# Kernel optimization log

Hardware: AMD Instinct MI355X
Metric: run time of the kernel (lower is better)

The kernel has to match this reference:

```python
import jax, jax.numpy as jnp
import numpy as np
from jax import lax

B, N, D = 2, 2048, 1024
H = 16
DH = D // H
EXP = 4
INNER = EXP * D
KS = 3
POWER = 2
LN_EPS = 1e-5


def _layer_norm(x, g, b):
    mu = jnp.mean(x, axis=-1, keepdims=True)
    var = jnp.mean(jnp.square(x - mu), axis=-1, keepdims=True)
    return (x - mu) * lax.rsqrt(var + LN_EPS) * g + b


def setup_inputs() -> dict:
    key = jax.random.key(0)
    ks = jax.random.split(key, 12)
    s = 1.0 / np.sqrt(D)
    si = 1.0 / np.sqrt(INNER)
    return {
        "Q_in": jax.random.normal(ks[0], (B, N, D), jnp.float32),
        "X": jax.random.normal(ks[1], (B, N, D), jnp.float32),
        "Wq": jax.random.normal(ks[2], (D, D), jnp.float32) * s,
        "Wk": jax.random.normal(ks[3], (D, D), jnp.float32) * s,
        "Wv": jax.random.normal(ks[4], (D, D), jnp.float32) * s,
        "Wo": jax.random.normal(ks[5], (D, D), jnp.float32) * s,
        "Wup": jax.random.normal(ks[6], (D, 2 * INNER), jnp.float32) * s,
        "conv_w": jax.random.normal(ks[7], (INNER, 1, KS), jnp.float32) * 0.5,
        "Wdown": jax.random.normal(ks[8], (INNER, D), jnp.float32) * si,
        "g1": jnp.ones((D,), jnp.float32),
        "b1": jnp.zeros((D,), jnp.float32),
        "g2": jnp.ones((D,), jnp.float32),
        "b2": jnp.zeros((D,), jnp.float32),
        "dt": jnp.float32(0.1),
    }


def reference(Q_in, X, Wq, Wk, Wv, Wo, Wup, conv_w, Wdown, g1, b1, g2, b2, dt):
    Bn, Nn, d = Q_in.shape
    # --- attention path: kernelized quadratic attention (relu^power) ---
    Hc = _layer_norm(Q_in, g1, b1) + X                     # [B,N,d]
    def heads(x):
        return x.reshape(Bn, Nn, H, DH).transpose(0, 2, 1, 3)  # [B,H,N,dh]
    Qp = heads(Hc @ Wq)
    Kp = heads(Hc @ Wk)
    Vp = heads(Hc @ Wv)
    PhiQ = jax.nn.elu(Qp) + 1.0
    PhiK = jax.nn.elu(Kp) + 1.0
    W = jnp.einsum("bhnd,bhmd->bhnm", PhiQ, PhiK)          # [B,H,N,N]
    W = jnp.maximum(W, 0.0) ** POWER
    Attr = jnp.einsum("bhnm,bhmd->bhnd", W, Vp)
    Norm = jnp.sum(W, axis=-1, keepdims=True) + 1.0
    m = Attr / Norm - Vp                                   # [B,H,N,dh]
    m_concat = m.transpose(0, 2, 1, 3).reshape(Bn, Nn, d)
    dt_safe = jax.nn.softplus(dt)
    Q_interact = Q_in + dt_safe * (m_concat @ Wo)
    # --- gated depthwise-conv FFN (ConvSwiGLU) ---
    Qn2 = _layer_norm(Q_interact, g2, b2)
    GU = Qn2 @ Wup                                         # [B,N,2*INNER]
    G, U = GU[..., :INNER], GU[..., INNER:]
    Hf = jax.nn.silu(G) * U                                # [B,N,INNER]
    Hf_t = Hf.transpose(0, 2, 1)                           # [B,INNER,N]
    pad = (KS - 1) // 2
    Hc_t = lax.conv_general_dilated(
        Hf_t, conv_w, window_strides=(1,), padding=[(pad, pad)],
        dimension_numbers=("NCH", "OIH", "NCH"), feature_group_count=INNER)
    H_out = Hc_t.transpose(0, 2, 1) @ Wdown
    return Q_interact + H_out
```

## Files before the change

### kernel.cpp

```cpp
#include <hip/hip_runtime.h>

typedef unsigned short u16;
typedef __attribute__((ext_vector_type(8))) __bf16 bf16x8;
typedef __attribute__((ext_vector_type(4))) float f32x4;
typedef __attribute__((ext_vector_type(8))) unsigned short us8v;

__device__ __forceinline__ u16 f2bf(float x){
  union { float f; unsigned u; } v; v.f = x;
  unsigned r = v.u + 0x7fffu + ((v.u >> 16) & 1u);
  return (u16)(r >> 16);
}
__device__ __forceinline__ float bf2f(u16 h){
  union { unsigned u; float f; } v; v.u = ((unsigned)h) << 16;
  return v.f;
}
__device__ __forceinline__ void gld16(const void* g, void* l){
  __builtin_amdgcn_global_load_lds((const __attribute__((address_space(1))) unsigned int*)g,
                                   (__attribute__((address_space(3))) unsigned int*)l, 16, 0, 0);
}

__global__ __launch_bounds__(256) void tr_cvt(const float* __restrict__ S, u16* __restrict__ D,
                                              int R, int C){
  __shared__ float t[32][33];
  int c0 = blockIdx.x*32, r0 = blockIdx.y*32;
  int tx = threadIdx.x, ty = threadIdx.y;
  #pragma unroll
  for (int j=0;j<32;j+=8) t[ty+j][tx] = S[(size_t)(r0+ty+j)*C + (c0+tx)];
  __syncthreads();
  #pragma unroll
  for (int j=0;j<32;j+=8) D[(size_t)(c0+ty+j)*R + (r0+tx)] = f2bf(t[tx][ty+j]);
}

__global__ __launch_bounds__(256) void tr_cvt_up(const float* __restrict__ S, u16* __restrict__ D){
  __shared__ float t[32][33];
  int c0 = blockIdx.x*32, r0 = blockIdx.y*32;
  int tx = threadIdx.x, ty = threadIdx.y;
  #pragma unroll
  for (int j=0;j<32;j+=8) t[ty+j][tx] = S[(size_t)(r0+ty+j)*8192 + (c0+tx)];
  __syncthreads();
  #pragma unroll
  for (int j=0;j<32;j+=8){
    int c = c0 + ty + j;
    int rdst = (c < 4096) ? ((c>>4)*32 + (c&15)) : (((c-4096)>>4)*32 + 16 + (c&15));
    D[(size_t)rdst*1024 + (r0+tx)] = f2bf(t[tx][ty+j]);
  }
}

__global__ __launch_bounds__(256) void ln_kernel(const float* __restrict__ Q, const float* __restrict__ X,
    const float* __restrict__ g, const float* __restrict__ b, u16* __restrict__ O){
  int row = blockIdx.x, tid = threadIdx.x;
  const float4 x = ((const float4*)(Q + (size_t)row*1024))[tid];
  float s = x.x + x.y + x.z + x.w;
  float sq = x.x*x.x + x.y*x.y + x.z*x.z + x.w*x.w;
  #pragma unroll
  for (int o=32;o>0;o>>=1){ s += __shfl_xor(s, o); sq += __shfl_xor(sq, o); }
  __shared__ float ss[4], ssq[4];
  int wid = tid>>6;
  if ((tid&63)==0){ ss[wid]=s; ssq[wid]=sq; }
  __syncthreads();
  s = ss[0]+ss[1]+ss[2]+ss[3]; sq = ssq[0]+ssq[1]+ssq[2]+ssq[3];
  float mu = s*(1.0f/1024.0f);
  float var = sq*(1.0f/1024.0f) - mu*mu;
  float rstd = rsqrtf(var + 1e-5f);
  float4 xx = make_float4(0.f,0.f,0.f,0.f);
  if (X) xx = ((const float4*)(X + (size_t)row*1024))[tid];
  float4 gv = ((const float4*)g)[tid];
  float4 bv = ((const float4*)b)[tid];
  ushort4 o;
  o.x = f2bf((x.x-mu)*rstd*gv.x + bv.x + xx.x);
  o.y = f2bf((x.y-mu)*rstd*gv.y + bv.y + xx.y);
  o.z = f2bf((x.z-mu)*rstd*gv.z + bv.z + xx.z);
  o.w = f2bf((x.w-mu)*rstd*gv.w + bv.w + xx.w);
  ((ushort4*)(O + (size_t)row*1024))[tid] = o;
}

__global__ __launch_bounds__(256) void ln2_kernel(const float* __restrict__ P,
    const float* __restrict__ Qin, const float* __restrict__ dtp,
    const float* __restrict__ g, const float* __restrict__ b,
    float* __restrict__ Qint, u16* __restrict__ Qn2){
  int row = blockIdx.x, tid = threadIdx.x;
  float sp = log1pf(__expf(dtp[0]));
  size_t off = (size_t)row*1024;
  float4 p0 = ((const float4*)(P + off))[tid];
  float4 p1 = ((const float4*)(P + 4194304 + off))[tid];
  float4 q  = ((const float4*)(Qin + off))[tid];
  float4 x;
  x.x = q.x + sp*(p0.x+p1.x); x.y = q.y + sp*(p0.y+p1.y);
  x.z = q.z + sp*(p0.z+p1.z); x.w = q.w + sp*(p0.w+p1.w);
  ((float4*)(Qint + off))[tid] = x;
  float s = x.x + x.y + x.z + x.w;
  float sq = x.x*x.x + x.y*x.y + x.z*x.z + x.w*x.w;
  #pragma unroll
  for (int o=32;o>0;o>>=1){ s += __shfl_xor(s, o); sq += __shfl_xor(sq, o); }
  __shared__ float ss[4], ssq[4];
  int wid = tid>>6;
  if ((tid&63)==0){ ss[wid]=s; ssq[wid]=sq; }
  __syncthreads();
  s = ss[0]+ss[1]+ss[2]+ss[3]; sq = ssq[0]+ssq[1]+ssq[2]+ssq[3];
  float mu = s*(1.0f/1024.0f);
  float var = sq*(1.0f/1024.0f) - mu*mu;
  float rstd = rsqrtf(var + 1e-5f);
  float4 gv = ((const float4*)g)[tid];
  float4 bv = ((const float4*)b)[tid];
  ushort4 o;
  o.x = f2bf((x.x-mu)*rstd*gv.x + bv.x);
  o.y = f2bf((x.y-mu)*rstd*gv.y + bv.y);
  o.z = f2bf((x.z-mu)*rstd*gv.z + bv.z);
  o.w = f2bf((x.w-mu)*rstd*gv.w + bv.w);
  ((ushort4*)(Qn2 + off))[tid] = o;
}

template<int EPI>
__global__ __launch_bounds__(256, 3) void gemm_bt(
    const u16* __restrict__ A, const u16* __restrict__ Bt,
    int M, int Nc, int K,
    void* __restrict__ Op, const float* __restrict__ aux, const float* __restrict__ dtp)
{
  __shared__ u16 As[128*32];
  __shared__ u16 Bs[128*32];
  const int tid = threadIdx.x, wid = tid>>6, lane = tid&63;
  const int g = lane>>4, l = lane&15;
  const int row0 = blockIdx.x*128, col0 = blockIdx.y*128;
  const int wr = (wid&1)*64, wc = (wid>>1)*64;
  const int l3 = l & 3;
  f32x4 acc[4][4] = {};
  for (int k0 = 0; k0 < K; k0 += 32){
    __syncthreads();
    #pragma unroll
    for (int i=0;i<2;i++){
      int ch0 = i*256 + wid*64;
      int ch = ch0 + lane;
      int r = ch >> 2, c = ch & 3;
      int cs = c ^ (r & 3);
      gld16(A  + (size_t)(row0+r)*K + k0 + cs*8, (char*)As + ch0*16);
      gld16(Bt + (size_t)(col0+r)*K + k0 + cs*8, (char*)Bs + ch0*16);
    }
    __syncthreads();
    bf16x8 a[4], b[4];
    #pragma unroll
    for (int i=0;i<4;i++) a[i] = *(const bf16x8*)(As + (wr + i*16 + l)*32 + (g^l3)*8);
    #pragma unroll
    for (int j=0;j<4;j++) b[j] = *(const bf16x8*)(Bs + (wc + j*16 + l)*32 + (g^l3)*8);
    #pragma unroll
    for (int i=0;i<4;i++)
      #pragma unroll
      for (int j=0;j<4;j++)
        acc[i][j] = __builtin_amdgcn_mfma_f32_16x16x32_bf16(a[i], b[j], acc[i][j], 0, 0, 0);
  }
  if constexpr (EPI == 6){
    #pragma unroll
    for (int i=0;i<4;i++)
     #pragma unroll
     for (int jj=0;jj<4;jj+=2)
      #pragma unroll
      for (int r=0;r<4;r++){
        int row = row0 + wr + i*16 + g*4 + r;
        int pair = (col0 + wc + jj*16) >> 5;
        float G = acc[i][jj][r], U = acc[i][jj+1][r];
        float hf = G/(1.f+__expf(-G))*U;
        ((u16*)Op)[(size_t)row*4096 + pair*16 + l] = f2bf(hf);
      }
  } else {
    #pragma unroll
    for (int i=0;i<4;i++)
     #pragma unroll
     for (int j=0;j<4;j++)
      #pragma unroll
      for (int r=0;r<4;r++){
        int row = row0 + wr + i*16 + g*4 + r;
        int col = col0 + wc + j*16 + l;
        float v = acc[i][j][r];
        int qk = col >> 10, c = col & 1023;
        int bb = row >> 11, n = row & 2047, h = c >> 6, d = c & 63;
        u16* P = (u16*)Op;
        if (qk == 2){
          P[(size_t)8388608 + (((size_t)(bb*16 + h))*64 + d)*2048 + n] = f2bf(v);
        } else {
          float phi = v > 0.f ? v + 1.f : __expf(v);
          P[(size_t)qk*4194304 + (((size_t)(bb*16 + h))*2048 + n)*64 + d] = f2bf(phi);
        }
      }
  }
}

__global__ __launch_bounds__(256, 3) void gemm_part(
    const u16* __restrict__ A, const u16* __restrict__ Bt,
    int Nc, int K, int Ks, float* __restrict__ Op)
{
  __shared__ u16 As[128*32];
  __shared__ u16 Bs[128*32];
  const int tid = threadIdx.x, wid = tid>>6, lane = tid&63;
  const int g = lane>>4, l = lane&15;
  const int row0 = blockIdx.x*128, col0 = blockIdx.y*128;
  const int kbase = blockIdx.z*Ks;
  const int wr = (wid&1)*64, wc = (wid>>1)*64;
  const int l3 = l & 3;
  f32x4 acc[4][4] = {};
  for (int k0 = kbase; k0 < kbase + Ks; k0 += 32){
    __syncthreads();
    #pragma unroll
    for (int i=0;i<2;i++){
      int ch0 = i*256 + wid*64;
      int ch = ch0 + lane;
      int r = ch >> 2, c = ch & 3;
      int cs = c ^ (r & 3);
      gld16(A  + (size_t)(row0+r)*K + k0 + cs*8, (char*)As + ch0*16);
      gld16(Bt + (size_t)(col0+r)*K + k0 + cs*8, (char*)Bs + ch0*16);
    }
    __syncthreads();
    bf16x8 a[4], b[4];
    #pragma unroll
    for (int i=0;i<4;i++) a[i] = *(const bf16x8*)(As + (wr + i*16 + l)*32 + (g^l3)*8);
    #pragma unroll
    for (int j=0;j<4;j++) b[j] = *(const bf16x8*)(Bs + (wc + j*16 + l)*32 + (g^l3)*8);
    #pragma unroll
    for (int i=0;i<4;i++)
      #pragma unroll
      for (int j=0;j<4;j++)
        acc[i][j] = __builtin_amdgcn_mfma_f32_16x16x32_bf16(a[i], b[j], acc[i][j], 0, 0, 0);
  }
  float* P = Op + (size_t)blockIdx.z*4194304;
  #pragma unroll
  for (int i=0;i<4;i++)
   #pragma unroll
   for (int j=0;j<4;j++)
    #pragma unroll
    for (int r=0;r<4;r++){
      int row = row0 + wr + i*16 + g*4 + r;
      int col = col0 + wc + j*16 + l;
      P[(size_t)row*Nc + col] = acc[i][j][r];
    }
}

__global__ __launch_bounds__(256) void reduce_out(const float* __restrict__ Qint,
    const float* __restrict__ P, float* __restrict__ out){
  size_t i = (size_t)blockIdx.x*256 + threadIdx.x;
  float4 a  = ((const float4*)Qint)[i];
  float4 p0 = ((const float4*)P)[i];
  float4 p1 = ((const float4*)(P + 4194304))[i];
  float4 o;
  o.x = a.x + p0.x + p1.x; o.y = a.y + p0.y + p1.y;
  o.z = a.z + p0.z + p1.z; o.w = a.w + p0.w + p1.w;
  ((float4*)out)[i] = o;
}

__global__ __launch_bounds__(256, 2) void attn_kernel(
    const u16* __restrict__ PhiQ, const u16* __restrict__ PhiK,
    const u16* __restrict__ Vt, u16* __restrict__ Mb)
{
  __shared__ u16 sQ[2][128][32];
  __shared__ u16 sK[2][128][32];
  __shared__ u16 sV[4][64][32];
  __shared__ u16 sW[128*128];
  const int tid = threadIdx.x, wid = tid>>6, lane = tid&63;
  const int g = lane>>4, l = lane&15;
  const int l3 = l & 3;
  const int q0 = blockIdx.x*128, bh = blockIdx.y;
  const u16* Q  = PhiQ + (size_t)bh*2048*64;
  const u16* Kb = PhiK + (size_t)bh*2048*64;
  const u16* V  = Vt   + (size_t)bh*64*2048;
  #pragma unroll
  for (int ks=0; ks<2; ks++)
    #pragma unroll
    for (int i=0;i<2;i++){
      int ch0 = i*256 + wid*64;
      int ch = ch0 + lane;
      int r = ch >> 2, q = ch & 3;
      int qs = q ^ (r & 3);
      gld16(Q + (size_t)(q0+r)*64 + ks*32 + qs*8, (char*)&sQ[ks][0][0] + ch0*16);
    }
  f32x4 accO[2][4] = {};
  float rsum[8] = {0.f,0.f,0.f,0.f,0.f,0.f,0.f,0.f};
  for (int m0 = 0; m0 < 2048; m0 += 128){
    __syncthreads();
    #pragma unroll
    for (int ks=0; ks<2; ks++)
      #pragma unroll
      for (int i=0;i<2;i++){
        int ch0 = i*256 + wid*64;
        int ch = ch0 + lane;
        int r = ch >> 2, q = ch & 3;
        int qs = q ^ (r & 3);
        gld16(Kb + (size_t)(m0+r)*64 + ks*32 + qs*8, (char*)&sK[ks][0][0] + ch0*16);
      }
    #pragma unroll
    for (int c=0; c<4; c++){
      int ch0 = wid*64;
      int ch = ch0 + lane;
      int d = ch >> 2, q = ch & 3;
      int qs = q ^ (d & 3);
      gld16(V + (size_t)d*2048 + m0 + c*32 + qs*8, (char*)&sV[c][0][0] + ch0*16);
    }
    __syncthreads();
    f32x4 st[2][8] = {};
    bf16x8 ak[2][2];
    #pragma unroll
    for (int rt=0;rt<2;rt++)
      #pragma unroll
      for (int ks=0;ks<2;ks++)
        ak[rt][ks] = *(const bf16x8*)&sK[ks][wid*32 + rt*16 + l][(g^l3)*8];
    #pragma unroll
    for (int ct=0;ct<8;ct++){
      #pragma unroll
      for (int ks=0;ks<2;ks++){
        bf16x8 bq = *(const bf16x8*)&sQ[ks][ct*16 + l][(g^l3)*8];
        st[0][ct] = __builtin_amdgcn_mfma_f32_16x16x32_bf16(ak[0][ks], bq, st[0][ct], 0,0,0);
        st[1][ct] = __builtin_amdgcn_mfma_f32_16x16x32_bf16(ak[1][ks], bq, st[1][ct], 0,0,0);
      }
    }
    #pragma unroll
    for (int ct=0;ct<8;ct++){
      float part = 0.f;
      #pragma unroll
      for (int rt=0;rt<2;rt++){
        float s0 = fmaxf(st[rt][ct][0], 0.f), s1 = fmaxf(st[rt][ct][1], 0.f);
        float s2 = fmaxf(st[rt][ct][2], 0.f), s3 = fmaxf(st[rt][ct][3], 0.f);
        float w0 = s0*s0, w1 = s1*s1, w2 = s2*s2, w3 = s3*s3;
        part += w0 + w1 + w2 + w3;
        int n = ct*16 + l;
        int mblk = wid*4 + rt*2 + (g>>1);
        ushort4 w4;
        w4.x = f2bf(w0); w4.y = f2bf(w1); w4.z = f2bf(w2); w4.w = f2bf(w3);
        *(ushort4*)(sW + n*128 + ((mblk ^ l)*8) + (g&1)*4) = w4;
      }
      rsum[ct] += part;
    }
    __syncthreads();
    #pragma unroll
    for (int ks=0;ks<4;ks++){
      int n0 = wid*32 + l, n1 = wid*32 + 16 + l;
      bf16x8 aw0 = *(const bf16x8*)(sW + n0*128 + (((ks*4+g) ^ (n0&15))*8));
      bf16x8 aw1 = *(const bf16x8*)(sW + n1*128 + (((ks*4+g) ^ (n1&15))*8));
      #pragma unroll
      for (int ct=0;ct<4;ct++){
        bf16x8 bv = *(const bf16x8*)&sV[ks][ct*16 + l][(g^l3)*8];
        accO[0][ct] = __builtin_amdgcn_mfma_f32_16x16x32_bf16(aw0, bv, accO[0][ct], 0,0,0);
        accO[1][ct] = __builtin_amdgcn_mfma_f32_16x16x32_bf16(aw1, bv, accO[1][ct], 0,0,0);
      }
    }
  }
  __syncthreads();
  float* sRS = (float*)sW;
  float* sNorm = ((float*)sW) + 512;
  #pragma unroll
  for (int ct=0;ct<8;ct++){
    float v = rsum[ct];
    v += __shfl_xor(v, 16);
    v += __shfl_xor(v, 32);
    rsum[ct] = v;
  }
  if (g == 0){
    #pragma unroll
    for (int ct=0;ct<8;ct++) sRS[wid*128 + ct*16 + l] = rsum[ct];
  }
  __syncthreads();
  if (tid < 128) sNorm[tid] = sRS[tid] + sRS[128+tid] + sRS[256+tid] + sRS[384+tid] + 1.0f;
  __syncthreads();
  const int bb = bh >> 4, h = bh & 15;
  #pragma unroll
  for (int rt=0;rt<2;rt++)
   #pragma unroll
   for (int ct=0;ct<4;ct++)
    #pragma unroll
    for (int r=0;r<4;r++){
      int n = wid*32 + rt*16 + g*4 + r;
      int d = ct*16 + l;
      float norm = sNorm[n];
      float vv = bf2f(V[(size_t)d*2048 + q0 + n]);
      float mv = accO[rt][ct][r]/norm - vv;
      Mb[((size_t)(bb*2048) + q0 + n)*1024 + h*64 + d] = f2bf(mv);
    }
}

__global__ __launch_bounds__(256) void conv_kernel(const u16* __restrict__ Hf, const float* __restrict__ w,
                                                   u16* __restrict__ Cv){
  int row = blockIdx.y;
  int n = row & 2047;
  int c0 = (blockIdx.x*256 + threadIdx.x)*8;
  us8v h0 = {0,0,0,0,0,0,0,0}, h2 = {0,0,0,0,0,0,0,0};
  us8v h1 = *(const us8v*)(Hf + (size_t)row*4096 + c0);
  if (n > 0)    h0 = *(const us8v*)(Hf + (size_t)(row-1)*4096 + c0);
  if (n < 2047) h2 = *(const us8v*)(Hf + (size_t)(row+1)*4096 + c0);
  us8v o;
  #pragma unroll
  for (int e=0;e<8;e++){
    int c = c0 + e;
    float acc = bf2f(h0[e])*w[c*3+0] + bf2f(h1[e])*w[c*3+1] + bf2f(h2[e])*w[c*3+2];
    o[e] = f2bf(acc);
  }
  *(us8v*)(Cv + (size_t)row*4096 + c0) = o;
}

extern "C" void kernel_launch(void* const* d_in, const int* in_sizes, int n_in,
                              void* d_out, int out_size, void* d_ws, size_t ws_size,
                              hipStream_t stream)
{
  const float* Q_in  = (const float*)d_in[0];
  const float* X     = (const float*)d_in[1];
  const float* Wq    = (const float*)d_in[2];
  const float* Wk    = (const float*)d_in[3];
  const float* Wv    = (const float*)d_in[4];
  const float* Wo    = (const float*)d_in[5];
  const float* Wup   = (const float*)d_in[6];
  const float* convw = (const float*)d_in[7];
  const float* Wdown = (const float*)d_in[8];
  const float* g1    = (const float*)d_in[9];
  const float* b1    = (const float*)d_in[10];
  const float* g2    = (const float*)d_in[11];
  const float* b2    = (const float*)d_in[12];
  const float* dt    = (const float*)d_in[13];
  float* out = (float*)d_out;

  char* ws = (char*)d_ws;
  const size_t MB = (size_t)1 << 20;
  u16* HcB   = (u16*)(ws + 0*MB);
  u16* WqkvT = (u16*)(ws + 8*MB);
  u16* WoT   = (u16*)(ws + 14*MB);
  u16* PhiQ  = (u16*)(ws + 16*MB);
  u16* Vt    = (u16*)(ws + 32*MB);
  u16* Mb    = (u16*)(ws + 40*MB);
  float* Po  = (float*)(ws + 48*MB);
  u16* WupT  = (u16*)(ws + 80*MB);
  u16* WdT   = (u16*)(ws + 96*MB);
  float* Qint = (float*)(ws + 104*MB);
  u16* Qn2   = (u16*)(ws + 120*MB);
  u16* Hf    = (u16*)(ws + 0*MB);
  u16* Cv    = (u16*)(ws + 40*MB);
  float* Pd  = (float*)(ws + 0*MB);
  u16* PhiK  = PhiQ + 4194304;

  dim3 tb(32, 8);
  tr_cvt<<<dim3(32, 32),  tb, 0, stream>>>(Wq,    WqkvT,               1024, 1024);
  tr_cvt<<<dim3(32, 32),  tb, 0, stream>>>(Wk,    WqkvT + 1024*1024,   1024, 1024);
  tr_cvt<<<dim3(32, 32),  tb, 0, stream>>>(Wv,    WqkvT + 2*1024*1024, 1024, 1024);
  tr_cvt<<<dim3(32, 32),  tb, 0, stream>>>(Wo,    WoT, 1024, 1024);
  tr_cvt_up<<<dim3(256, 32), tb, 0, stream>>>(Wup, WupT);
  tr_cvt<<<dim3(32, 128), tb, 0, stream>>>(Wdown, WdT, 4096, 1024);

  ln_kernel<<<4096, 256, 0, stream>>>(Q_in, X, g1, b1, HcB);

  gemm_bt<5><<<dim3(32, 24), 256, 0, stream>>>(HcB, WqkvT, 4096, 3072, 1024, PhiQ, nullptr, nullptr);

  attn_kernel<<<dim3(16, 32), 256, 0, stream>>>(PhiQ, PhiK, Vt, Mb);

  gemm_part<<<dim3(32, 8, 2), 256, 0, stream>>>(Mb, WoT, 1024, 1024, 512, Po);

  ln2_kernel<<<4096, 256, 0, stream>>>(Po, Q_in, dt, g2, b2, Qint, Qn2);

  gemm_bt<6><<<dim3(32, 64), 256, 0, stream>>>(Qn2, WupT, 4096, 8192, 1024, Hf, nullptr, nullptr);

  conv_kernel<<<dim3(2, 4096), 256, 0, stream>>>(Hf, convw, Cv);

  gemm_part<<<dim3(32, 8, 2), 256, 0, stream>>>(Cv, WdT, 1024, 4096, 2048, Pd);
  reduce_out<<<4096, 256, 0, stream>>>(Qint, Pd, out);
}
```

Measured before the change: 449.0 us.

## Use wider 256x128 tile GEMM with grouped block order for up-projection

Replaces the generic 128x128-tile GEMM for the Wup projection with a dedicated kernel using 256x128 tiles (each wave computes 128x64), and remaps the 1D block index so groups of row tiles share column tiles for better L2 reuse. The SwiGLU epilogue is kept, and the old EPI==6 branch is removed from the generic GEMM. The larger tile raises the MFMA-to-LDS-load ratio and halves B-tile refetches, at the cost of more registers, lower occupancy (launch bound 2), and no overlap between global loads and compute.

Result: no change. 451.6 us (+0.6%).

```diff
diff --git a/kernel.cpp b/kernel.cpp
--- a/kernel.cpp
+++ b/kernel.cpp
@@ -147,40 +147,82 @@
       for (int j=0;j<4;j++)
         acc[i][j] = __builtin_amdgcn_mfma_f32_16x16x32_bf16(a[i], b[j], acc[i][j], 0, 0, 0);
   }
-  if constexpr (EPI == 6){
-    #pragma unroll
-    for (int i=0;i<4;i++)
-     #pragma unroll
-     for (int jj=0;jj<4;jj+=2)
-      #pragma unroll
-      for (int r=0;r<4;r++){
-        int row = row0 + wr + i*16 + g*4 + r;
-        int pair = (col0 + wc + jj*16) >> 5;
-        float G = acc[i][jj][r], U = acc[i][jj+1][r];
-        float hf = G/(1.f+__expf(-G))*U;
-        ((u16*)Op)[(size_t)row*4096 + pair*16 + l] = f2bf(hf);
+  #pragma unroll
+  for (int i=0;i<4;i++)
+   #pragma unroll
+   for (int j=0;j<4;j++)
+    #pragma unroll
+    for (int r=0;r<4;r++){
+      int row = row0 + wr + i*16 + g*4 + r;
+      int col = col0 + wc + j*16 + l;
+      float v = acc[i][j][r];
+      int qk = col >> 10, c = col & 1023;
+      int bb = row >> 11, n = row & 2047, h = c >> 6, d = c & 63;
+      u16* P = (u16*)Op;
+      if (qk == 2){
+        P[(size_t)8388608 + (((size_t)(bb*16 + h))*64 + d)*2048 + n] = f2bf(v);
+      } else {
+        float phi = v > 0.f ? v + 1.f : __expf(v);
+        P[(size_t)qk*4194304 + (((size_t)(bb*16 + h))*2048 + n)*64 + d] = f2bf(phi);
       }
-  } else {
-    #pragma unroll
-    for (int i=0;i<4;i++)
-     #pragma unroll
-     for (int j=0;j<4;j++)
-      #pragma unroll
-      for (int r=0;r<4;r++){
-        int row = row0 + wr + i*16 + g*4 + r;
-        int col = col0 + wc + j*16 + l;
-        float v = acc[i][j][r];
-        int qk = col >> 10, c = col & 1023;
-        int bb = row >> 11, n = row & 2047, h = c >> 6, d = c & 63;
-        u16* P = (u16*)Op;
-        if (qk == 2){
-          P[(size_t)8388608 + (((size_t)(bb*16 + h))*64 + d)*2048 + n] = f2bf(v);
-        } else {
-          float phi = v > 0.f ? v + 1.f : __expf(v);
-          P[(size_t)qk*4194304 + (((size_t)(bb*16 + h))*2048 + n)*64 + d] = f2bf(phi);
-        }
-      }
-  }
+    }
+}
+
+__global__ __launch_bounds__(256, 2) void gemm_wide_up(
+    const u16* __restrict__ A, const u16* __restrict__ Bt, u16* __restrict__ Op)
+{
+  __shared__ u16 As[256*32];
+  __shared__ u16 Bs[128*32];
+  const int tid = threadIdx.x, wid = tid>>6, lane = tid&63;
+  const int g = lane>>4, l = lane&15, l3 = l&3;
+  const int bid = blockIdx.x;
+  const int bx = bid & 15;
+  const int by = (bid>>7)*8 + ((bid>>4) & 7);
+  const int row0 = bx*256, col0 = by*128;
+  const int wr = (wid&1)*128, wc = (wid>>1)*64;
+  f32x4 acc[8][4] = {};
+  for (int k0 = 0; k0 < 1024; k0 += 32){
+    __syncthreads();
+    #pragma unroll
+    for (int i=0;i<4;i++){
+      int ch0 = i*256 + wid*64;
+      int ch = ch0 + lane;
+      int r = ch >> 2, c = ch & 3;
+      int cs = c ^ (r & 3);
+      gld16(A + (size_t)(row0+r)*1024 + k0 + cs*8, (char*)As + ch0*16);
+    }
+    #pragma unroll
+    for (int i=0;i<2;i++){
+      int ch0 = i*256 + wid*64;
+      int ch = ch0 + lane;
+      int r = ch >> 2, c = ch & 3;
+      int cs = c ^ (r & 3);
+      gld16(Bt + (size_t)(col0+r)*1024 + k0 + cs*8, (char*)Bs + ch0*16);
+    }
+    __syncthreads();
+    bf16x8 a[8], b[4];
+    #pragma unroll
+    for (int i=0;i<8;i++) a[i] = *(const bf16x8*)(As + (wr + i*16 + l)*32 + (g^l3)*8);
+    #pragma unroll
+    for (int j=0;j<4;j++) b[j] = *(const bf16x8*)(Bs + (wc + j*16 + l)*32 + (g^l3)*8);
+    #pragma unroll
+    for (int i=0;i<8;i++)
+      #pragma unroll
+      for (int j=0;j<4;j++)
+        acc[i][j] = __builtin_amdgcn_mfma_f32_16x16x32_bf16(a[i], b[j], acc[i][j], 0, 0, 0);
+  }
+  #pragma unroll
+  for (int i=0;i<8;i++)
+   #pragma unroll
+   for (int jj=0;jj<4;jj+=2)
+    #pragma unroll
+    for (int r=0;r<4;r++){
+      int row = row0 + wr + i*16 + g*4 + r;
+      int pair = (col0 + wc + jj*16) >> 5;
+      float G = acc[i][jj][r], U = acc[i][jj+1][r];
+      float hf = G/(1.f+__expf(-G))*U;
+      Op[(size_t)row*4096 + pair*16 + l] = f2bf(hf);
+    }
 }
 
 __global__ __launch_bounds__(256, 3) void gemm_part(
@@ -447,7 +489,7 @@
 
   ln2_kernel<<<4096, 256, 0, stream>>>(Po, Q_in, dt, g2, b2, Qint, Qn2);
 
-  gemm_bt<6><<<dim3(32, 64), 256, 0, stream>>>(Qn2, WupT, 4096, 8192, 1024, Hf, nullptr, nullptr);
+  gemm_wide_up<<<1024, 256, 0, stream>>>(Qn2, WupT, Hf);
 
   conv_kernel<<<dim3(2, 4096), 256, 0, stream>>>(Hf, convw, Cv);
 
```
